# Kernel tuning notes

Measured on AMD Instinct MI355X. Metric: run time of the kernel, lower is better.

Reference implementation:

```python
import jax, jax.numpy as jnp
import numpy as np

EPS = 1e-5

def conv3x3(x, W, b):
    # NCHW 3x3 conv, padding=1 (SAME)
    y = jax.lax.conv_general_dilated(x, W, (1, 1), ((1, 1), (1, 1)),
                                     dimension_numbers=('NCHW', 'OIHW', 'NCHW'))
    return y + b[None, :, None, None]

def bn_relu(x, gamma, beta):
    # BatchNorm2d in training mode: batch statistics over (N,H,W)
    m = x.mean(axis=(0, 2, 3), keepdims=True)
    v = x.var(axis=(0, 2, 3), keepdims=True)
    xn = (x - m) * jax.lax.rsqrt(v + EPS)
    return jax.nn.relu(xn * gamma[None, :, None, None] + beta[None, :, None, None])

def haar_dwt2(x):
    # pywt.dwt2(x, 'db1') for even H,W: cA=LL, cH=row-detail/col-approx,
    # cV=row-approx/col-detail, cD=HH; each 0.5*(+-a +-b +-c +-d)
    a = x[:, :, 0::2, 0::2]
    b = x[:, :, 0::2, 1::2]
    c = x[:, :, 1::2, 0::2]
    d = x[:, :, 1::2, 1::2]
    cA = (a + b + c + d) * 0.5
    cH = (a + b - c - d) * 0.5
    cV = (a - b + c - d) * 0.5
    cD = (a - b - c + d) * 0.5
    return jnp.concatenate([cA, cH, cV, cD], axis=1)  # [B, 4C, H/2, W/2]

def setup_inputs() -> dict:
    key = jax.random.key(0)
    ks = jax.random.split(key, 4)
    B, Cin, Cout, H, W = 8, 64, 128, 256, 256
    inputs = jax.random.normal(ks[0], (B, Cin, H, W), dtype=jnp.float32)
    W1 = jax.random.normal(ks[1], (Cout, Cin, 3, 3), dtype=jnp.float32) * 0.05
    W2 = jax.random.normal(ks[2], (Cout, Cout, 3, 3), dtype=jnp.float32) * 0.05
    W3 = jax.random.normal(ks[3], (Cout, 4 * Cout, 3, 3), dtype=jnp.float32) * 0.05
    z = jnp.zeros((Cout,), jnp.float32)
    o = jnp.ones((Cout,), jnp.float32)
    return {"inputs": inputs,
            "W1": W1, "b1": z, "g1": o, "be1": z,
            "W2": W2, "b2": z, "g2": o, "be2": z,
            "W3": W3, "b3": z, "g3": o, "be3": z}

def reference(inputs, W1, b1, g1, be1, W2, b2, g2, be2, W3, b3, g3, be3):
    h = bn_relu(conv3x3(inputs, W1, b1), g1, be1)
    skip_con = bn_relu(conv3x3(h, W2, b2), g2, be2)          # [B, out_c, H, W]
    # original detaches before the pywt round-trip
    dwt = haar_dwt2(jax.lax.stop_gradient(skip_con))          # [B, 4*out_c, H/2, W/2]
    dwt_out = bn_relu(conv3x3(dwt, W3, b3), g3, be3)          # [B, out_c, H/2, W/2]
    return (skip_con, dwt_out)
```

## Files before the change

kernel.cpp:

```cpp
#include <hip/hip_runtime.h>

typedef __attribute__((ext_vector_type(8))) short bf16x8;
typedef __attribute__((ext_vector_type(4))) short bf16x4;
typedef __attribute__((ext_vector_type(4))) float f32x4;

__device__ __forceinline__ float bf2f(ushort u) {
  union { unsigned int i; float f; } v; v.i = ((unsigned int)u) << 16; return v.f;
}
__device__ __forceinline__ ushort f2bf(float f) {
  union { float f; unsigned int i; } v; v.f = f;
  unsigned int x = v.i;
  unsigned int r = (x + 0x7fffu + ((x >> 16) & 1u)) >> 16;
  return (ushort)r;
}

__global__ void zero_f32(float* p, int n) {
  int i = blockIdx.x * 256 + threadIdx.x;
  if (i < n) p[i] = 0.f;
}

__global__ void pack_w(const float* __restrict__ W, ushort* __restrict__ Wp, int Cin) {
  int ncic = Cin >> 5;
  int total = 9 * ncic * 8 * 64 * 8;
  for (int idx = blockIdx.x * 256 + threadIdx.x; idx < total; idx += gridDim.x * 256) {
    int j = idx & 7;
    int l = (idx >> 3) & 63;
    int cf = (idx >> 9) & 7;
    int rest = idx >> 12;
    int cic = rest % ncic;
    int tap = rest / ncic;
    int co = cf * 16 + (l & 15);
    int ci = cic * 32 + ((l >> 4) * 8) + j;
    int ky = tap / 3, kx = tap % 3;
    Wp[idx] = f2bf(W[((co * Cin + ci) * 3 + ky) * 3 + kx]);
  }
}

__global__ __launch_bounds__(256)
void nchw2nhwc(const float* __restrict__ in, ushort* __restrict__ out) {
  const int n  = blockIdx.y;
  const int p0 = blockIdx.x << 6;
  const int tid = threadIdx.x;
  __shared__ ushort t[64 * 72];
  {
    int c  = tid >> 2;
    int pq = (tid & 3) << 4;
    const float* ip = in + (((size_t)(n * 64 + c)) << 16) + p0 + pq;
#pragma unroll
    for (int k = 0; k < 4; ++k) {
      float4 f = *(const float4*)(ip + k * 4);
      int p = pq + k * 4;
      t[(p + 0) * 72 + c] = f2bf(f.x);
      t[(p + 1) * 72 + c] = f2bf(f.y);
      t[(p + 2) * 72 + c] = f2bf(f.z);
      t[(p + 3) * 72 + c] = f2bf(f.w);
    }
  }
  __syncthreads();
#pragma unroll
  for (int k = 0; k < 2; ++k) {
    int id = k * 256 + tid;
    int cj = id & 7, p = id >> 3;
    bf16x8 v = *(const bf16x8*)&t[p * 72 + cj * 8];
    *(bf16x8*)(out + ((((size_t)n << 16) + p0 + p) << 6) + cj * 8) = v;
  }
}

__device__ __forceinline__ bf16x8 bnrelu8(bf16x8 v, const float* __restrict__ coef, int c0) {
  float4 a0 = *(const float4*)(coef + c0);
  float4 a1 = *(const float4*)(coef + c0 + 4);
  float4 b0 = *(const float4*)(coef + 128 + c0);
  float4 b1 = *(const float4*)(coef + 128 + c0 + 4);
  bf16x8 r;
  r[0] = (short)f2bf(fmaxf(a0.x * bf2f((ushort)v[0]) + b0.x, 0.f));
  r[1] = (short)f2bf(fmaxf(a0.y * bf2f((ushort)v[1]) + b0.y, 0.f));
  r[2] = (short)f2bf(fmaxf(a0.z * bf2f((ushort)v[2]) + b0.z, 0.f));
  r[3] = (short)f2bf(fmaxf(a0.w * bf2f((ushort)v[3]) + b0.w, 0.f));
  r[4] = (short)f2bf(fmaxf(a1.x * bf2f((ushort)v[4]) + b1.x, 0.f));
  r[5] = (short)f2bf(fmaxf(a1.y * bf2f((ushort)v[5]) + b1.y, 0.f));
  r[6] = (short)f2bf(fmaxf(a1.z * bf2f((ushort)v[6]) + b1.z, 0.f));
  r[7] = (short)f2bf(fmaxf(a1.w * bf2f((ushort)v[7]) + b1.w, 0.f));
  return r;
}

template<int MODE>
__global__ __launch_bounds__(512, 4)
void conv_mfma(const ushort* __restrict__ src, const ushort* __restrict__ Wp,
               const float* __restrict__ bias, const float* __restrict__ coef,
               ushort* __restrict__ out, float* __restrict__ sSum, float* __restrict__ sSsq,
               int Cin, int H, int W)
{
  const int ncic = Cin >> 5;
  const int x0 = blockIdx.x << 6;
  const int y0 = blockIdx.y << 1;
  const int n  = blockIdx.z;
  const int tid = threadIdx.x;
  const int wv = tid >> 6, l = tid & 63, l15 = l & 15, l4 = l >> 4;
  const int cg = wv >> 1;
  const int wy = wv & 1;

  __shared__ __align__(16) ushort smem[2 * 8448];

  const size_t HW = (size_t)H * W;
  const ushort* srcn = src + (size_t)n * HW * Cin;

  int off[3];
#pragma unroll
  for (int it = 0; it < 3; ++it) {
    int i = it * 512 + tid;
    int cj = i & 3, p = i >> 2;
    int row = p / 66, xt = p - row * 66;
    int ry = y0 + row - 1, gx = x0 + xt - 1;
    bool ok = (i < 1056) && ((unsigned)ry < (unsigned)H) && ((unsigned)gx < (unsigned)W);
    off[it] = ok ? (int)((ry * W + gx) * Cin + (cj << 3)) : -1;
  }

  f32x4 acc[2][4];
#pragma unroll
  for (int f = 0; f < 2; ++f)
#pragma unroll
    for (int xf = 0; xf < 4; ++xf) acc[f][xf] = (f32x4){0.f, 0.f, 0.f, 0.f};

  bf16x8 st[3];

  auto LOADREG = [&](int cic) {
#pragma unroll
    for (int it = 0; it < 3; ++it) {
      bf16x8 v = {};
      if (off[it] >= 0) v = *(const bf16x8*)(srcn + off[it] + (cic << 5));
      st[it] = v;
    }
  };

  auto WRITE = [&](ushort* buf, int cic) {
#pragma unroll
    for (int it = 0; it < 3; ++it) {
      if (it < 2 || tid < 32) {
        int i = it * 512 + tid;
        bf16x8 v = st[it];
        if (MODE == 1) {
          if (off[it] >= 0) v = bnrelu8(v, coef, (cic << 5) + ((i & 3) << 3));
        }
        *(bf16x8*)(buf + i * 8) = v;
      }
    }
  };

  auto COMPUTE = [&](const ushort* buf, int cic) {
    const ushort* wp = Wp + ((size_t)cic * 8 + (cg << 1)) * 512 + ((size_t)l << 3);
    const size_t tstride = (size_t)ncic * 4096;
    const ushort* lrow = buf + (size_t)l15 * 32 + (l4 << 3);
#pragma unroll
    for (int tap = 0; tap < 9; ++tap) {
      const int ky = tap / 3, kx = tap % 3;
      bf16x8 a0 = *(const bf16x8*)(wp + (size_t)tap * tstride);
      bf16x8 a1 = *(const bf16x8*)(wp + (size_t)tap * tstride + 512);
      bf16x8 b[4];
#pragma unroll
      for (int xf = 0; xf < 4; ++xf)
        b[xf] = *(const bf16x8*)(lrow + (((wy + ky) * 66 + (xf << 4) + kx) << 5));
#pragma unroll
      for (int xf = 0; xf < 4; ++xf) {
        acc[0][xf] = __builtin_amdgcn_mfma_f32_16x16x32_bf16(a0, b[xf], acc[0][xf], 0, 0, 0);
        acc[1][xf] = __builtin_amdgcn_mfma_f32_16x16x32_bf16(a1, b[xf], acc[1][xf], 0, 0, 0);
      }
    }
  };

  LOADREG(0);
  WRITE(smem, 0);
  __syncthreads();

  int cur = 0;
  for (int cic = 0; cic < ncic; ++cic) {
    if (cic + 1 < ncic) LOADREG(cic + 1);
    COMPUTE(smem + cur * 8448, cic);
    if (cic + 1 < ncic) WRITE(smem + (cur ^ 1) * 8448, cic + 1);
    __syncthreads();
    cur ^= 1;
  }

  float smv[2][4] = {{0.f}}, sqv[2][4] = {{0.f}};
  ushort* eps = smem;
  for (int yr = 0; yr < 2; ++yr) {
    __syncthreads();
    if (wy == yr) {
#pragma unroll
      for (int f = 0; f < 2; ++f) {
        const int col = (cg << 5) + (f << 4) + (l4 << 2);
        float4 bv = *(const float4*)(bias + col);
#pragma unroll
        for (int xf = 0; xf < 4; ++xf) {
          float v0 = acc[f][xf][0] + bv.x;
          float v1 = acc[f][xf][1] + bv.y;
          float v2 = acc[f][xf][2] + bv.z;
          float v3 = acc[f][xf][3] + bv.w;
          smv[f][0] += v0; sqv[f][0] += v0 * v0;
          smv[f][1] += v1; sqv[f][1] += v1 * v1;
          smv[f][2] += v2; sqv[f][2] += v2 * v2;
          smv[f][3] += v3; sqv[f][3] += v3 * v3;
          bf16x4 u;
          u[0] = (short)f2bf(v0); u[1] = (short)f2bf(v1);
          u[2] = (short)f2bf(v2); u[3] = (short)f2bf(v3);
          *(bf16x4*)&eps[((xf << 4) + l15) * 136 + col] = u;
        }
      }
    }
    __syncthreads();
    {
      const int xx = tid >> 3, c0 = (tid & 7) << 4;
      ushort* op = out + ((size_t)n * HW + (size_t)(y0 + yr) * W + x0 + xx) * 128 + c0;
      *(bf16x8*)op       = *(const bf16x8*)&eps[xx * 136 + c0];
      *(bf16x8*)(op + 8) = *(const bf16x8*)&eps[xx * 136 + c0 + 8];
    }
  }

  const int rep = (int)((blockIdx.z * gridDim.y + blockIdx.y) * gridDim.x + blockIdx.x) & 31;
#pragma unroll
  for (int f = 0; f < 2; ++f)
#pragma unroll
    for (int j = 0; j < 4; ++j) {
      float s = smv[f][j], q = sqv[f][j];
#pragma unroll
      for (int o = 1; o < 16; o <<= 1) { s += __shfl_xor(s, o); q += __shfl_xor(q, o); }
      if (l15 == 0) {
        int co = (cg << 5) + (f << 4) + (l4 << 2) + j;
        atomicAdd(&sSum[rep * 128 + co], s);
        atomicAdd(&sSsq[rep * 128 + co], q);
      }
    }
}

__global__ void bn_finalize(const float* __restrict__ sSum, const float* __restrict__ sSsq,
                            const float* __restrict__ g, const float* __restrict__ be,
                            float* __restrict__ coef, float invN)
{
  int c = threadIdx.x;
  float S = 0.f, Q = 0.f;
  for (int r = 0; r < 32; ++r) { S += sSum[r * 128 + c]; Q += sSsq[r * 128 + c]; }
  float m = S * invN;
  float v = Q * invN - m * m;
  float a = g[c] / sqrtf(v + 1e-5f);
  coef[c] = a;
  coef[128 + c] = be[c] - m * a;
}

__global__ __launch_bounds__(256)
void skip_dwt2(const ushort* __restrict__ skipRaw, const float* __restrict__ coef,
               float* __restrict__ outSkip, ushort* __restrict__ dwt)
{
  const int x0 = blockIdx.x << 6;
  const int oy = blockIdx.y;
  const int n  = blockIdx.z >> 2;
  const int ct = blockIdx.z & 3;
  const int y0 = oy << 1;
  const int tid = threadIdx.x;
  __shared__ float t32[32 * 2 * 68];

#pragma unroll
  for (int it = 0; it < 2; ++it) {
    int i = it * 256 + tid;
    int cj = i & 3, x = (i >> 2) & 63, r = i >> 8;
    int c0 = (ct << 5) + (cj << 3);
    bf16x8 v = *(const bf16x8*)(skipRaw + (((size_t)n << 16) + (size_t)(y0 + r) * 256 + x0 + x) * 128 + c0);
    float4 a0 = *(const float4*)(coef + c0);
    float4 a1 = *(const float4*)(coef + c0 + 4);
    float4 b0 = *(const float4*)(coef + 128 + c0);
    float4 b1 = *(const float4*)(coef + 128 + c0 + 4);
    float av[8] = {a0.x, a0.y, a0.z, a0.w, a1.x, a1.y, a1.z, a1.w};
    float bv[8] = {b0.x, b0.y, b0.z, b0.w, b1.x, b1.y, b1.z, b1.w};
    int cl = cj << 3;
#pragma unroll
    for (int k = 0; k < 8; ++k)
      t32[((cl + k) * 2 + r) * 68 + x] = fmaxf(av[k] * bf2f((ushort)v[k]) + bv[k], 0.f);
  }
  __syncthreads();

  {
    int c = tid >> 3, x8 = (tid & 7) << 3;
    float* op = outSkip + (((size_t)(n * 128 + (ct << 5) + c)) << 16) + (size_t)y0 * 256 + x0 + x8;
#pragma unroll
    for (int r = 0; r < 2; ++r) {
      float4 r0 = *(const float4*)&t32[(c * 2 + r) * 68 + x8];
      float4 r1 = *(const float4*)&t32[(c * 2 + r) * 68 + x8 + 4];
      *(float4*)(op + (size_t)r * 256) = r0;
      *(float4*)(op + (size_t)r * 256 + 4) = r1;
    }
  }

  if (tid < 128) {
    int cj = tid & 3, ox = tid >> 2;
    int cl = cj << 3;
    bf16x8 oA, oH, oV, oD;
#pragma unroll
    for (int k = 0; k < 8; ++k) {
      int c = cl + k;
      float p00 = t32[(c * 2 + 0) * 68 + 2 * ox];
      float p01 = t32[(c * 2 + 0) * 68 + 2 * ox + 1];
      float p10 = t32[(c * 2 + 1) * 68 + 2 * ox];
      float p11 = t32[(c * 2 + 1) * 68 + 2 * ox + 1];
      oA[k] = (short)f2bf((p00 + p01 + p10 + p11) * 0.5f);
      oH[k] = (short)f2bf((p00 + p01 - p10 - p11) * 0.5f);
      oV[k] = (short)f2bf((p00 - p01 + p10 - p11) * 0.5f);
      oD[k] = (short)f2bf((p00 - p01 - p10 + p11) * 0.5f);
    }
    size_t db = ((size_t)n * 16384 + (size_t)oy * 128 + (x0 >> 1) + ox) * 512 + (ct << 5) + cl;
    *(bf16x8*)(dwt + db)       = oA;
    *(bf16x8*)(dwt + db + 128) = oH;
    *(bf16x8*)(dwt + db + 256) = oV;
    *(bf16x8*)(dwt + db + 384) = oD;
  }
}

__global__ __launch_bounds__(256)
void bn_transpose_out(const ushort* __restrict__ src, const float* __restrict__ coef,
                      float* __restrict__ dst, int H, int W)
{
  const int n  = blockIdx.z >> 2;
  const int cc = blockIdx.z & 3;
  const int x0 = blockIdx.x << 6;
  const int y  = blockIdx.y;
  const int tid = threadIdx.x;
  __shared__ float t[32 * 68];
  const size_t HW = (size_t)H * W;
  {
    int p = tid >> 2, cj = tid & 3;
    int c0 = (cc << 5) + (cj << 3);
    bf16x8 v = *(const bf16x8*)(src + ((size_t)n * HW + (size_t)y * W + x0 + p) * 128 + c0);
    float4 a0 = *(const float4*)(coef + c0);
    float4 a1 = *(const float4*)(coef + c0 + 4);
    float4 b0 = *(const float4*)(coef + 128 + c0);
    float4 b1 = *(const float4*)(coef + 128 + c0 + 4);
    int cl = cj << 3;
    t[(cl + 0) * 68 + p] = fmaxf(a0.x * bf2f((ushort)v[0]) + b0.x, 0.f);
    t[(cl + 1) * 68 + p] = fmaxf(a0.y * bf2f((ushort)v[1]) + b0.y, 0.f);
    t[(cl + 2) * 68 + p] = fmaxf(a0.z * bf2f((ushort)v[2]) + b0.z, 0.f);
    t[(cl + 3) * 68 + p] = fmaxf(a0.w * bf2f((ushort)v[3]) + b0.w, 0.f);
    t[(cl + 4) * 68 + p] = fmaxf(a1.x * bf2f((ushort)v[4]) + b1.x, 0.f);
    t[(cl + 5) * 68 + p] = fmaxf(a1.y * bf2f((ushort)v[5]) + b1.y, 0.f);
    t[(cl + 6) * 68 + p] = fmaxf(a1.z * bf2f((ushort)v[6]) + b1.z, 0.f);
    t[(cl + 7) * 68 + p] = fmaxf(a1.w * bf2f((ushort)v[7]) + b1.w, 0.f);
  }
  __syncthreads();
  {
    int c = tid >> 3, x8 = (tid & 7) << 3;
    float4 r0 = *(const float4*)&t[c * 68 + x8];
    float4 r1 = *(const float4*)&t[c * 68 + x8 + 4];
    float* op = dst + ((size_t)(n * 128 + (cc << 5) + c)) * HW + (size_t)y * W + x0 + x8;
    *(float4*)op = r0;
    *(float4*)(op + 4) = r1;
  }
}

extern "C" void kernel_launch(void* const* d_in, const int* in_sizes, int n_in,
                              void* d_out, int out_size, void* d_ws, size_t ws_size,
                              hipStream_t stream)
{
  const float* input = (const float*)d_in[0];
  const float* W1  = (const float*)d_in[1];
  const float* b1  = (const float*)d_in[2];
  const float* g1  = (const float*)d_in[3];
  const float* be1 = (const float*)d_in[4];
  const float* W2  = (const float*)d_in[5];
  const float* b2  = (const float*)d_in[6];
  const float* g2  = (const float*)d_in[7];
  const float* be2 = (const float*)d_in[8];
  const float* W3  = (const float*)d_in[9];
  const float* b3  = (const float*)d_in[10];
  const float* g3  = (const float*)d_in[11];
  const float* be3 = (const float*)d_in[12];

  char* ws = (char*)d_ws;
  ushort* h_raw    = (ushort*)(ws + 0);
  ushort* skip_raw = (ushort*)(ws + 134217728);
  ushort* dwt      = (ushort*)(ws + 268435456);
  ushort* in_nhwc  = (ushort*)(ws + 268435456);
  ushort* raw3     = (ushort*)(ws + 402653184);
  float*  stats    = (float*)(ws + 436207616);
  float*  s1 = stats,          *q1 = stats + 4096;
  float*  s2 = stats + 8192,   *q2 = stats + 12288;
  float*  s3 = stats + 16384,  *q3 = stats + 20480;
  float*  coef = (float*)(ws + 436305920);
  float*  c1 = coef, *c2 = coef + 256, *c3 = coef + 512;
  ushort* Wp1 = (ushort*)(ws + 436308992);
  ushort* Wp2 = (ushort*)(ws + 436456448);
  ushort* Wp3 = (ushort*)(ws + 436751360);

  zero_f32<<<96, 256, 0, stream>>>(stats, 24576);
  pack_w<<<288, 256, 0, stream>>>(W1, Wp1, 64);
  pack_w<<<576, 256, 0, stream>>>(W2, Wp2, 128);
  pack_w<<<2304, 256, 0, stream>>>(W3, Wp3, 512);
  nchw2nhwc<<<dim3(1024, 8), 256, 0, stream>>>(input, in_nhwc);

  conv_mfma<0><<<dim3(4, 128, 8), 512, 0, stream>>>(in_nhwc, Wp1, b1, nullptr,
                                                    h_raw, s1, q1, 64, 256, 256);
  bn_finalize<<<1, 128, 0, stream>>>(s1, q1, g1, be1, c1, 1.f / 524288.f);

  conv_mfma<1><<<dim3(4, 128, 8), 512, 0, stream>>>(h_raw, Wp2, b2, c1,
                                                    skip_raw, s2, q2, 128, 256, 256);
  bn_finalize<<<1, 128, 0, stream>>>(s2, q2, g2, be2, c2, 1.f / 524288.f);

  skip_dwt2<<<dim3(4, 128, 32), 256, 0, stream>>>(skip_raw, c2, (float*)d_out, dwt);

  conv_mfma<0><<<dim3(2, 64, 8), 512, 0, stream>>>(dwt, Wp3, b3, nullptr,
                                                   raw3, s3, q3, 512, 128, 128);
  bn_finalize<<<1, 128, 0, stream>>>(s3, q3, g3, be3, c3, 1.f / 131072.f);

  bn_transpose_out<<<dim3(2, 128, 32), 256, 0, stream>>>(raw3, c3, (float*)d_out + 67108864, 128, 128);
}
```

Measured before the change: 744.5 us.

## Switch conv to 32x32x16 MFMA with 4-row tiles and channel-split LDS layout

The implicit-GEMM conv kernel moves from 16x16x32 to 32x32x16 bf16 MFMA instructions. Each block now computes 4 output rows instead of 2, and the weight packing is reordered to match the new operand layout. The LDS tile is stored channel-chunk-major so B-operand lanes read consecutive pixels, and BN statistics are reduced and atomically added inside the epilogue. The aim is fewer MFMA and LDS instructions per FLOP and more input reuse per block, at the cost of more LDS, more accumulator registers and a zero-fill pass for border blocks.

```diff
diff --git a/kernel.cpp b/kernel.cpp
--- a/kernel.cpp
+++ b/kernel.cpp
@@ -2,7 +2,7 @@
 
 typedef __attribute__((ext_vector_type(8))) short bf16x8;
 typedef __attribute__((ext_vector_type(4))) short bf16x4;
-typedef __attribute__((ext_vector_type(4))) float f32x4;
+typedef __attribute__((ext_vector_type(16))) float f32x16;
 
 __device__ __forceinline__ float bf2f(ushort u) {
   union { unsigned int i; float f; } v; v.i = ((unsigned int)u) << 16; return v.f;
@@ -21,16 +21,17 @@
 
 __global__ void pack_w(const float* __restrict__ W, ushort* __restrict__ Wp, int Cin) {
   int ncic = Cin >> 5;
-  int total = 9 * ncic * 8 * 64 * 8;
+  int total = 9 * ncic * 2 * 4 * 64 * 8;
   for (int idx = blockIdx.x * 256 + threadIdx.x; idx < total; idx += gridDim.x * 256) {
     int j = idx & 7;
     int l = (idx >> 3) & 63;
-    int cf = (idx >> 9) & 7;
+    int cf = (idx >> 9) & 3;
+    int ks = (idx >> 11) & 1;
     int rest = idx >> 12;
     int cic = rest % ncic;
     int tap = rest / ncic;
-    int co = cf * 16 + (l & 15);
-    int ci = cic * 32 + ((l >> 4) * 8) + j;
+    int co = (cf << 5) + (l & 31);
+    int ci = (cic << 5) + (ks << 4) + ((l >> 5) << 3) + j;
     int ky = tap / 3, kx = tap % 3;
     Wp[idx] = f2bf(W[((co * Cin + ci) * 3 + ky) * 3 + kx]);
   }
@@ -92,40 +93,44 @@
 {
   const int ncic = Cin >> 5;
   const int x0 = blockIdx.x << 6;
-  const int y0 = blockIdx.y << 1;
+  const int y0 = blockIdx.y << 2;
   const int n  = blockIdx.z;
   const int tid = threadIdx.x;
-  const int wv = tid >> 6, l = tid & 63, l15 = l & 15, l4 = l >> 4;
-  const int cg = wv >> 1;
-  const int wy = wv & 1;
-
-  __shared__ __align__(16) ushort smem[2 * 8448];
+  const int wv = tid >> 6, l = tid & 63, l31 = l & 31, lh = l >> 5;
+  const int cg  = wv >> 2;
+  const int pxg = wv & 3;
+
+  __shared__ __align__(16) ushort smem[2 * 1584 * 8];
 
   const size_t HW = (size_t)H * W;
   const ushort* srcn = src + (size_t)n * HW * Cin;
 
-  int off[3];
-#pragma unroll
-  for (int it = 0; it < 3; ++it) {
+  int off[4], wch[4];
+#pragma unroll
+  for (int it = 0; it < 4; ++it) {
     int i = it * 512 + tid;
     int cj = i & 3, p = i >> 2;
     int row = p / 66, xt = p - row * 66;
     int ry = y0 + row - 1, gx = x0 + xt - 1;
-    bool ok = (i < 1056) && ((unsigned)ry < (unsigned)H) && ((unsigned)gx < (unsigned)W);
+    bool ok = (i < 1584) && ((unsigned)ry < (unsigned)H) && ((unsigned)gx < (unsigned)W);
     off[it] = ok ? (int)((ry * W + gx) * Cin + (cj << 3)) : -1;
-  }
-
-  f32x4 acc[2][4];
-#pragma unroll
-  for (int f = 0; f < 2; ++f)
-#pragma unroll
-    for (int xf = 0; xf < 4; ++xf) acc[f][xf] = (f32x4){0.f, 0.f, 0.f, 0.f};
-
-  bf16x8 st[3];
+    wch[it] = row * 264 + cj * 66 + xt;
+  }
+
+  if (x0 == 0 || x0 + 64 >= W || y0 == 0 || y0 + 4 >= H) {
+    for (int k = tid; k < 3168; k += 512) *(bf16x8*)&smem[k << 3] = (bf16x8){};
+  }
+  __syncthreads();
+
+  f32x16 acc[2][2];
+  acc[0][0] = f32x16{}; acc[0][1] = f32x16{};
+  acc[1][0] = f32x16{}; acc[1][1] = f32x16{};
+
+  bf16x8 st[4];
 
   auto LOADREG = [&](int cic) {
 #pragma unroll
-    for (int it = 0; it < 3; ++it) {
+    for (int it = 0; it < 4; ++it) {
       bf16x8 v = {};
       if (off[it] >= 0) v = *(const bf16x8*)(srcn + off[it] + (cic << 5));
       st[it] = v;
@@ -134,35 +139,37 @@
 
   auto WRITE = [&](ushort* buf, int cic) {
 #pragma unroll
-    for (int it = 0; it < 3; ++it) {
-      if (it < 2 || tid < 32) {
+    for (int it = 0; it < 4; ++it) {
+      if (it < 3 || tid < 48) {
         int i = it * 512 + tid;
         bf16x8 v = st[it];
         if (MODE == 1) {
           if (off[it] >= 0) v = bnrelu8(v, coef, (cic << 5) + ((i & 3) << 3));
         }
-        *(bf16x8*)(buf + i * 8) = v;
+        *(bf16x8*)(buf + (wch[it] << 3)) = v;
       }
     }
   };
 
   auto COMPUTE = [&](const ushort* buf, int cic) {
-    const ushort* wp = Wp + ((size_t)cic * 8 + (cg << 1)) * 512 + ((size_t)l << 3);
+    const ushort* wpc = Wp + (size_t)cic * 4096 + (size_t)(cg << 1) * 512 + ((size_t)l << 3);
     const size_t tstride = (size_t)ncic * 4096;
-    const ushort* lrow = buf + (size_t)l15 * 32 + (l4 << 3);
+    const ushort* bl = buf + (((size_t)lh * 66 + l31) << 3);
 #pragma unroll
     for (int tap = 0; tap < 9; ++tap) {
       const int ky = tap / 3, kx = tap % 3;
-      bf16x8 a0 = *(const bf16x8*)(wp + (size_t)tap * tstride);
-      bf16x8 a1 = *(const bf16x8*)(wp + (size_t)tap * tstride + 512);
-      bf16x8 b[4];
-#pragma unroll
-      for (int xf = 0; xf < 4; ++xf)
-        b[xf] = *(const bf16x8*)(lrow + (((wy + ky) * 66 + (xf << 4) + kx) << 5));
-#pragma unroll
-      for (int xf = 0; xf < 4; ++xf) {
-        acc[0][xf] = __builtin_amdgcn_mfma_f32_16x16x32_bf16(a0, b[xf], acc[0][xf], 0, 0, 0);
-        acc[1][xf] = __builtin_amdgcn_mfma_f32_16x16x32_bf16(a1, b[xf], acc[1][xf], 0, 0, 0);
+      const ushort* wpt = wpc + (size_t)tap * tstride;
+      const ushort* brow = bl + (((pxg + ky) * 264 + kx) << 3);
+#pragma unroll
+      for (int ks = 0; ks < 2; ++ks) {
+        bf16x8 a0 = *(const bf16x8*)(wpt + (ks << 11));
+        bf16x8 a1 = *(const bf16x8*)(wpt + (ks << 11) + 512);
+        bf16x8 b0 = *(const bf16x8*)(brow + (ks * 132 << 3));
+        bf16x8 b1 = *(const bf16x8*)(brow + ((ks * 132 + 32) << 3));
+        acc[0][0] = __builtin_amdgcn_mfma_f32_32x32x16_bf16(a0, b0, acc[0][0], 0, 0, 0);
+        acc[0][1] = __builtin_amdgcn_mfma_f32_32x32x16_bf16(a0, b1, acc[0][1], 0, 0, 0);
+        acc[1][0] = __builtin_amdgcn_mfma_f32_32x32x16_bf16(a1, b0, acc[1][0], 0, 0, 0);
+        acc[1][1] = __builtin_amdgcn_mfma_f32_32x32x16_bf16(a1, b1, acc[1][1], 0, 0, 0);
       }
     }
   };
@@ -174,35 +181,46 @@
   int cur = 0;
   for (int cic = 0; cic < ncic; ++cic) {
     if (cic + 1 < ncic) LOADREG(cic + 1);
-    COMPUTE(smem + cur * 8448, cic);
-    if (cic + 1 < ncic) WRITE(smem + (cur ^ 1) * 8448, cic + 1);
+    COMPUTE(smem + cur * 12672, cic);
+    if (cic + 1 < ncic) WRITE(smem + (cur ^ 1) * 12672, cic + 1);
     __syncthreads();
     cur ^= 1;
   }
 
-  float smv[2][4] = {{0.f}}, sqv[2][4] = {{0.f}};
   ushort* eps = smem;
-  for (int yr = 0; yr < 2; ++yr) {
+  const int rep = (int)((blockIdx.z * gridDim.y + blockIdx.y) * gridDim.x + blockIdx.x) & 31;
+  for (int yr = 0; yr < 4; ++yr) {
     __syncthreads();
-    if (wy == yr) {
+    if (pxg == yr) {
 #pragma unroll
       for (int f = 0; f < 2; ++f) {
-        const int col = (cg << 5) + (f << 4) + (l4 << 2);
-        float4 bv = *(const float4*)(bias + col);
-#pragma unroll
-        for (int xf = 0; xf < 4; ++xf) {
-          float v0 = acc[f][xf][0] + bv.x;
-          float v1 = acc[f][xf][1] + bv.y;
-          float v2 = acc[f][xf][2] + bv.z;
-          float v3 = acc[f][xf][3] + bv.w;
-          smv[f][0] += v0; sqv[f][0] += v0 * v0;
-          smv[f][1] += v1; sqv[f][1] += v1 * v1;
-          smv[f][2] += v2; sqv[f][2] += v2 * v2;
-          smv[f][3] += v3; sqv[f][3] += v3 * v3;
-          bf16x4 u;
-          u[0] = (short)f2bf(v0); u[1] = (short)f2bf(v1);
-          u[2] = (short)f2bf(v2); u[3] = (short)f2bf(v3);
-          *(bf16x4*)&eps[((xf << 4) + l15) * 136 + col] = u;
+#pragma unroll
+        for (int q = 0; q < 4; ++q) {
+          const int cob = (cg << 6) + (f << 5) + (q << 3) + (lh << 2);
+          float4 bv = *(const float4*)(bias + cob);
+          float v0[4], v1[4];
+#pragma unroll
+          for (int j = 0; j < 4; ++j) {
+            float b = (j == 0) ? bv.x : (j == 1) ? bv.y : (j == 2) ? bv.z : bv.w;
+            v0[j] = acc[f][0][q * 4 + j] + b;
+            v1[j] = acc[f][1][q * 4 + j] + b;
+          }
+          bf16x4 u0, u1;
+#pragma unroll
+          for (int j = 0; j < 4; ++j) { u0[j] = (short)f2bf(v0[j]); u1[j] = (short)f2bf(v1[j]); }
+          *(bf16x4*)&eps[l31 * 136 + cob] = u0;
+          *(bf16x4*)&eps[(32 + l31) * 136 + cob] = u1;
+#pragma unroll
+          for (int j = 0; j < 4; ++j) {
+            float s = v0[j] + v1[j];
+            float qq = v0[j] * v0[j] + v1[j] * v1[j];
+#pragma unroll
+            for (int o = 1; o <= 16; o <<= 1) { s += __shfl_xor(s, o); qq += __shfl_xor(qq, o); }
+            if (l31 == 0) {
+              atomicAdd(&sSum[rep * 128 + cob + j], s);
+              atomicAdd(&sSsq[rep * 128 + cob + j], qq);
+            }
+          }
         }
       }
     }
@@ -214,21 +232,6 @@
       *(bf16x8*)(op + 8) = *(const bf16x8*)&eps[xx * 136 + c0 + 8];
     }
   }
-
-  const int rep = (int)((blockIdx.z * gridDim.y + blockIdx.y) * gridDim.x + blockIdx.x) & 31;
-#pragma unroll
-  for (int f = 0; f < 2; ++f)
-#pragma unroll
-    for (int j = 0; j < 4; ++j) {
-      float s = smv[f][j], q = sqv[f][j];
-#pragma unroll
-      for (int o = 1; o < 16; o <<= 1) { s += __shfl_xor(s, o); q += __shfl_xor(q, o); }
-      if (l15 == 0) {
-        int co = (cg << 5) + (f << 4) + (l4 << 2) + j;
-        atomicAdd(&sSum[rep * 128 + co], s);
-        atomicAdd(&sSsq[rep * 128 + co], q);
-      }
-    }
 }
 
 __global__ void bn_finalize(const float* __restrict__ sSum, const float* __restrict__ sSsq,
@@ -392,17 +395,17 @@
   pack_w<<<2304, 256, 0, stream>>>(W3, Wp3, 512);
   nchw2nhwc<<<dim3(1024, 8), 256, 0, stream>>>(input, in_nhwc);
 
-  conv_mfma<0><<<dim3(4, 128, 8), 512, 0, stream>>>(in_nhwc, Wp1, b1, nullptr,
-                                                    h_raw, s1, q1, 64, 256, 256);
+  conv_mfma<0><<<dim3(4, 64, 8), 512, 0, stream>>>(in_nhwc, Wp1, b1, nullptr,
+                                                   h_raw, s1, q1, 64, 256, 256);
   bn_finalize<<<1, 128, 0, stream>>>(s1, q1, g1, be1, c1, 1.f / 524288.f);
 
-  conv_mfma<1><<<dim3(4, 128, 8), 512, 0, stream>>>(h_raw, Wp2, b2, c1,
-                                                    skip_raw, s2, q2, 128, 256, 256);
+  conv_mfma<1><<<dim3(4, 64, 8), 512, 0, stream>>>(h_raw, Wp2, b2, c1,
+                                                   skip_raw, s2, q2, 128, 256, 256);
   bn_finalize<<<1, 128, 0, stream>>>(s2, q2, g2, be2, c2, 1.f / 524288.f);
 
   skip_dwt2<<<dim3(4, 128, 32), 256, 0, stream>>>(skip_raw, c2, (float*)d_out, dwt);
 
-  conv_mfma<0><<<dim3(2, 64, 8), 512, 0, stream>>>(dwt, Wp3, b3, nullptr,
+  conv_mfma<0><<<dim3(2, 32, 8), 512, 0, stream>>>(dwt, Wp3, b3, nullptr,
                                                    raw3, s3, q3, 512, 128, 128);
   bn_finalize<<<1, 128, 0, stream>>>(s3, q3, g3, be3, c3, 1.f / 131072.f);
 
```

Result: slower. 1.264 ms (+69.7%).
